# Kernel tuning notes

Hardware: AMD Instinct MI355X
Metric: run time of the kernel (lower is better)

Reference implementation:

```python
import jax, jax.numpy as jnp
import numpy as np

D = 1024        # input_dim == hidden_dim (residual add requires equality)
NUM_CLASSES = 2
EPS = 1e-5      # torch LayerNorm default


def _layer_norm(x, gamma, beta):
    mu = jnp.mean(x, axis=-1, keepdims=True)
    var = jnp.var(x, axis=-1, keepdims=True)
    return (x - mu) * jax.lax.rsqrt(var + EPS) * gamma + beta


def setup_inputs() -> dict:
    key = jax.random.key(0)
    ks = jax.random.split(key, 16)
    B, S = 8, 2048
    s = 1.0 / np.sqrt(D)
    inp = {
        "x": jax.random.normal(ks[0], (B, S, D), dtype=jnp.float32),
        "Wq": jax.random.normal(ks[1], (D, D), dtype=jnp.float32) * s,
        "bq": jnp.zeros((D,), jnp.float32),
        "Wk": jax.random.normal(ks[2], (D, D), dtype=jnp.float32) * s,
        "bk": jnp.zeros((D,), jnp.float32),
        "Wv": jax.random.normal(ks[3], (D, D), dtype=jnp.float32) * s,
        "bv": jnp.zeros((D,), jnp.float32),
        "Wd": jax.random.normal(ks[4], (D, D), dtype=jnp.float32) * s,
        "bd": jnp.zeros((D,), jnp.float32),
        "g1": jnp.ones((D,), jnp.float32),
        "b1": jnp.zeros((D,), jnp.float32),
        "g2": jnp.ones((D,), jnp.float32),
        "b2": jnp.zeros((D,), jnp.float32),
        "Wc": jax.random.normal(ks[5], (D, NUM_CLASSES), dtype=jnp.float32) * s,
        "bc": jnp.zeros((NUM_CLASSES,), jnp.float32),
    }
    return inp


def reference(x, Wq, bq, Wk, bk, Wv, bv, Wd, bd, g1, b1, g2, b2, Wc, bc):
    # Q/K/V projections
    q = x @ Wq + bq                                   # [B,S,D]
    k = x @ Wk + bk
    v = x @ Wv + bv
    # scores scaled by sqrt(input_dim) (as in the original code)
    scores = jnp.einsum('bsd,btd->bst', q, k) / np.sqrt(D).astype(np.float32)
    attn = jax.nn.softmax(scores, axis=-1)            # [B,S,S]
    weighted = jnp.einsum('bst,btd->bsd', attn, v)    # [B,S,D]
    weighted = _layer_norm(weighted + x, g1, b1)
    h = jax.nn.relu(weighted @ Wd + bd)
    h = _layer_norm(h + weighted, g2, b2)
    # dropout is identity in eval mode
    logits = h[:, 0, :] @ Wc + bc                     # [B,num_classes]
    return logits
```

## Files before the change

### kernel.cpp

```cpp
#include <hip/hip_runtime.h>
#include <math.h>

#define B 8
#define S 2048
#define D 1024

__device__ __forceinline__ float waveReduceSum(float v) {
#pragma unroll
    for (int k = 32; k >= 1; k >>= 1) v += __shfl_xor(v, k, 64);
    return v;
}
__device__ __forceinline__ float waveReduceMax(float v) {
#pragma unroll
    for (int k = 32; k >= 1; k >>= 1) v = fmaxf(v, __shfl_xor(v, k, 64));
    return v;
}
__device__ float blockReduceSum(float v) {
    __shared__ float sm[4];
    int lane = threadIdx.x & 63, wid = threadIdx.x >> 6;
    v = waveReduceSum(v);
    __syncthreads();
    if (lane == 0) sm[wid] = v;
    __syncthreads();
    return sm[0] + sm[1] + sm[2] + sm[3];
}

__global__ void __launch_bounds__(256) k1_q0(const float* __restrict__ x,
                                             const float* __restrict__ Wq,
                                             const float* __restrict__ bq,
                                             float* __restrict__ q0,
                                             float* __restrict__ zero_region) {
    const int tid = threadIdx.x;
    zero_region[blockIdx.x * 256 + tid] = 0.f;

    const int dp0 = blockIdx.x * 16;
    const int dpl = tid & 15, kg = tid >> 4;
    __shared__ float xs[8][1024];
    for (int j = tid; j < 2048; j += 256) {
        int b = j >> 8, off = j & 255;
        ((float4*)xs[b])[off] = ((const float4*)(x + (size_t)b * S * D))[off];
    }
    __syncthreads();
    float acc[8] = {0.f, 0.f, 0.f, 0.f, 0.f, 0.f, 0.f, 0.f};
    const int k0 = kg * 64;
    for (int i = 0; i < 64; ++i) {
        int k = k0 + i;
        float wv = Wq[(size_t)k * D + dp0 + dpl];
#pragma unroll
        for (int b = 0; b < 8; ++b) acc[b] += xs[b][k] * wv;
    }
    __shared__ float red[16 * 16 * 9];
#pragma unroll
    for (int b = 0; b < 8; ++b) red[(kg * 16 + dpl) * 9 + b] = acc[b];
    __syncthreads();
    if (tid < 128) {
        int dpl2 = tid >> 3, b = tid & 7;
        float s = 0.f;
#pragma unroll
        for (int g = 0; g < 16; ++g) s += red[(g * 16 + dpl2) * 9 + b];
        q0[b * D + dp0 + dpl2] = s + bq[dp0 + dpl2];
    }
}

__global__ void __launch_bounds__(256) k2_u(const float* __restrict__ Wk,
                                            const float* __restrict__ q0,
                                            float* __restrict__ u) {
    int wid = (blockIdx.x * 256 + threadIdx.x) >> 6;
    int lane = threadIdx.x & 63;
    const float4* Wk4 = (const float4*)(Wk + (size_t)wid * D);
    const float4* q04 = (const float4*)q0;
    float acc[8] = {0.f, 0.f, 0.f, 0.f, 0.f, 0.f, 0.f, 0.f};
#pragma unroll
    for (int i = 0; i < 4; ++i) {
        float4 wv = Wk4[lane + 64 * i];
#pragma unroll
        for (int b = 0; b < 8; ++b) {
            float4 qv = q04[b * 256 + lane + 64 * i];
            acc[b] += wv.x * qv.x + wv.y * qv.y + wv.z * qv.z + wv.w * qv.w;
        }
    }
#pragma unroll
    for (int b = 0; b < 8; ++b) {
        float v = waveReduceSum(acc[b]);
        if (lane == 0) u[b * D + wid] = v;
    }
}

__global__ void __launch_bounds__(256) k3_attn(const float* __restrict__ x,
                                               const float* __restrict__ u,
                                               float* __restrict__ pml,
                                               float* __restrict__ pw) {
    const int b = blockIdx.y;
    const int t0 = blockIdx.x * 16;
    const int tid = threadIdx.x;
    const int wave = tid >> 6, lane = tid & 63;
    const float4* xb4 = (const float4*)(x + (size_t)b * S * D);
    float4 xr[16];
#pragma unroll
    for (int t = 0; t < 16; ++t) xr[t] = xb4[(size_t)(t0 + t) * 256 + tid];
    float4 uv = ((const float4*)(u + b * D))[tid];
    __shared__ float part[16][256];
#pragma unroll
    for (int t = 0; t < 16; ++t)
        part[t][tid] = xr[t].x * uv.x + xr[t].y * uv.y + xr[t].z * uv.z + xr[t].w * uv.w;
    __syncthreads();
    __shared__ float s_sc[16];
#pragma unroll
    for (int r = 0; r < 4; ++r) {
        int t = wave * 4 + r;
        float v = part[t][lane] + part[t][lane + 64] + part[t][lane + 128] + part[t][lane + 192];
        v = waveReduceSum(v);
        if (lane == 0) s_sc[t] = v * 0.03125f;
    }
    __syncthreads();
    float m = -INFINITY;
#pragma unroll
    for (int t = 0; t < 16; ++t) m = fmaxf(m, s_sc[t]);
    float p[16], l = 0.f;
#pragma unroll
    for (int t = 0; t < 16; ++t) {
        p[t] = __expf(s_sc[t] - m);
        l += p[t];
    }
    float4 wl = {0.f, 0.f, 0.f, 0.f};
#pragma unroll
    for (int t = 0; t < 16; ++t) {
        wl.x += p[t] * xr[t].x;
        wl.y += p[t] * xr[t].y;
        wl.z += p[t] * xr[t].z;
        wl.w += p[t] * xr[t].w;
    }
    const int pidx = b * 128 + blockIdx.x;
    ((float4*)(pw + (size_t)pidx * 1024))[tid] = wl;
    if (tid == 0) {
        pml[pidx * 2 + 0] = m;
        pml[pidx * 2 + 1] = l;
    }
}

__global__ void __launch_bounds__(256) k4_comb_wv(const float* __restrict__ pml,
                                                  const float* __restrict__ pw,
                                                  const float* __restrict__ Wv,
                                                  float* __restrict__ wacc) {
    const int tid = threadIdx.x;
    const int bid = blockIdx.x;
    const int d0 = (bid >> 2) * 32;
    const int dp = (bid & 3) * 256 + tid;
    const int wave = tid >> 6, lane = tid & 63;
    __shared__ float pm[8][128], pl[8][128], sc[8][128];
    __shared__ float sM[8], sL[8];
    __shared__ float vs[8][32];
    for (int j = tid; j < 1024; j += 256) {
        int b = j >> 7, blk = j & 127;
        pm[b][blk] = pml[(b * 128 + blk) * 2 + 0];
        pl[b][blk] = pml[(b * 128 + blk) * 2 + 1];
    }
    __syncthreads();
#pragma unroll
    for (int h = 0; h < 2; ++h) {
        int b = wave + h * 4;
        float mv = fmaxf(pm[b][lane], pm[b][lane + 64]);
        float M = waveReduceMax(mv);
        float lp = __expf(pm[b][lane] - M) * pl[b][lane] +
                   __expf(pm[b][lane + 64] - M) * pl[b][lane + 64];
        float L = waveReduceSum(lp);
        if (lane == 0) {
            sM[b] = M;
            sL[b] = L;
        }
    }
    __syncthreads();
    for (int j = tid; j < 1024; j += 256) {
        int b = j >> 7, blk = j & 127;
        sc[b][blk] = __expf(pm[b][blk] - sM[b]);
    }
    __syncthreads();
    {
        int b = tid >> 5, dd = tid & 31, d = d0 + dd;
        float acc = 0.f;
#pragma unroll 4
        for (int blk = 0; blk < 128; ++blk)
            acc += sc[b][blk] * pw[(size_t)(b * 128 + blk) * 1024 + d];
        vs[b][dd] = acc / sL[b];
    }
    __syncthreads();
    float acc[8] = {0.f, 0.f, 0.f, 0.f, 0.f, 0.f, 0.f, 0.f};
#pragma unroll 4
    for (int dd = 0; dd < 32; ++dd) {
        float wv = Wv[(size_t)(d0 + dd) * D + dp];
#pragma unroll
        for (int b = 0; b < 8; ++b) acc[b] += vs[b][dd] * wv;
    }
#pragma unroll
    for (int b = 0; b < 8; ++b) atomicAdd(&wacc[b * D + dp], acc[b]);
}

__global__ void __launch_bounds__(256) k5_ln1_wd(const float* __restrict__ wacc,
                                                 const float* __restrict__ bv,
                                                 const float* __restrict__ x,
                                                 const float* __restrict__ g1,
                                                 const float* __restrict__ b1,
                                                 const float* __restrict__ Wd,
                                                 float* __restrict__ hacc) {
    const int tid = threadIdx.x;
    const int bid = blockIdx.x;
    const int d0 = (bid >> 2) * 32;
    const int dp = (bid & 3) * 256 + tid;
    const int wave = tid >> 6, lane = tid & 63;
    __shared__ float sMu[8], sInv[8], vs[8][32];
    {
        const float4* wacc4 = (const float4*)wacc;
        const float4* bv4 = (const float4*)bv;
#pragma unroll
        for (int h = 0; h < 2; ++h) {
            int b = wave + h * 4;
            const float4* xb4r = (const float4*)(x + (size_t)b * S * D);
            float s = 0.f, ss = 0.f;
#pragma unroll
            for (int i = 0; i < 4; ++i) {
                int idx = lane + 64 * i;
                float4 wv = wacc4[b * 256 + idx];
                float4 bb = bv4[idx];
                float4 xv = xb4r[idx];
                float v0 = wv.x + bb.x + xv.x;
                float v1 = wv.y + bb.y + xv.y;
                float v2 = wv.z + bb.z + xv.z;
                float v3 = wv.w + bb.w + xv.w;
                s += v0 + v1 + v2 + v3;
                ss += v0 * v0 + v1 * v1 + v2 * v2 + v3 * v3;
            }
            s = waveReduceSum(s);
            ss = waveReduceSum(ss);
            if (lane == 0) {
                float mu = s * (1.0f / D);
                sMu[b] = mu;
                sInv[b] = rsqrtf(ss * (1.0f / D) - mu * mu + 1e-5f);
            }
        }
    }
    __syncthreads();
    {
        int b = tid >> 5, dd = tid & 31, d = d0 + dd;
        float v = wacc[b * D + d] + bv[d] + x[(size_t)b * S * D + d];
        vs[b][dd] = (v - sMu[b]) * sInv[b] * g1[d] + b1[d];
    }
    __syncthreads();
    float acc[8] = {0.f, 0.f, 0.f, 0.f, 0.f, 0.f, 0.f, 0.f};
#pragma unroll 4
    for (int dd = 0; dd < 32; ++dd) {
        float wv = Wd[(size_t)(d0 + dd) * D + dp];
#pragma unroll
        for (int b = 0; b < 8; ++b) acc[b] += vs[b][dd] * wv;
    }
#pragma unroll
    for (int b = 0; b < 8; ++b) atomicAdd(&hacc[b * D + dp], acc[b]);
}

__global__ void __launch_bounds__(256) k6_final(const float* __restrict__ wacc,
                                                const float* __restrict__ bv,
                                                const float* __restrict__ x,
                                                const float* __restrict__ g1,
                                                const float* __restrict__ b1,
                                                const float* __restrict__ hacc,
                                                const float* __restrict__ bd,
                                                const float* __restrict__ g2,
                                                const float* __restrict__ b2,
                                                const float* __restrict__ Wc,
                                                const float* __restrict__ bc,
                                                float* __restrict__ out) {
    const int b = blockIdx.x;
    const int tid = threadIdx.x;
    float r[4];
    float s = 0.f, ss = 0.f;
#pragma unroll
    for (int i = 0; i < 4; ++i) {
        int e = tid * 4 + i;
        float v = wacc[b * D + e] + bv[e] + x[(size_t)b * S * D + e];
        r[i] = v;
        s += v;
        ss += v * v;
    }
    s = blockReduceSum(s);
    ss = blockReduceSum(ss);
    float mu1 = s * (1.0f / D);
    float inv1 = rsqrtf(ss * (1.0f / D) - mu1 * mu1 + 1e-5f);
    float t[4];
    float s2 = 0.f, ss2 = 0.f;
#pragma unroll
    for (int i = 0; i < 4; ++i) {
        int e = tid * 4 + i;
        float ln1v = (r[i] - mu1) * inv1 * g1[e] + b1[e];
        float h = fmaxf(hacc[b * D + e] + bd[e], 0.f) + ln1v;
        t[i] = h;
        s2 += h;
        ss2 += h * h;
    }
    s2 = blockReduceSum(s2);
    ss2 = blockReduceSum(ss2);
    float mu2 = s2 * (1.0f / D);
    float inv2 = rsqrtf(ss2 * (1.0f / D) - mu2 * mu2 + 1e-5f);
    float p0 = 0.f, p1 = 0.f;
#pragma unroll
    for (int i = 0; i < 4; ++i) {
        int e = tid * 4 + i;
        float l2 = (t[i] - mu2) * inv2 * g2[e] + b2[e];
        p0 += l2 * Wc[e * 2 + 0];
        p1 += l2 * Wc[e * 2 + 1];
    }
    p0 = blockReduceSum(p0);
    p1 = blockReduceSum(p1);
    if (tid == 0) {
        out[b * 2 + 0] = p0 + bc[0];
        out[b * 2 + 1] = p1 + bc[1];
    }
}

extern "C" void kernel_launch(void* const* d_in, const int* in_sizes, int n_in,
                              void* d_out, int out_size, void* d_ws, size_t ws_size,
                              hipStream_t stream) {
    const float* x  = (const float*)d_in[0];
    const float* Wq = (const float*)d_in[1];
    const float* bq = (const float*)d_in[2];
    const float* Wk = (const float*)d_in[3];
    const float* Wv = (const float*)d_in[5];
    const float* bv = (const float*)d_in[6];
    const float* Wd = (const float*)d_in[7];
    const float* bd = (const float*)d_in[8];
    const float* g1 = (const float*)d_in[9];
    const float* b1 = (const float*)d_in[10];
    const float* g2 = (const float*)d_in[11];
    const float* b2 = (const float*)d_in[12];
    const float* Wc = (const float*)d_in[13];
    const float* bc = (const float*)d_in[14];
    float* out = (float*)d_out;

    float* ws   = (float*)d_ws;
    float* q0   = ws;
    float* u    = ws + 8192;
    float* wacc = ws + 16384;
    float* hacc = ws + 24576;
    float* pml  = ws + 32768;
    float* pw   = ws + 34816;

    k1_q0<<<64, 256, 0, stream>>>(x, Wq, bq, q0, wacc);
    k2_u<<<256, 256, 0, stream>>>(Wk, q0, u);
    k3_attn<<<dim3(128, 8), 256, 0, stream>>>(x, u, pml, pw);
    k4_comb_wv<<<128, 256, 0, stream>>>(pml, pw, Wv, wacc);
    k5_ln1_wd<<<128, 256, 0, stream>>>(wacc, bv, x, g1, b1, Wd, hacc);
    k6_final<<<8, 256, 0, stream>>>(wacc, bv, x, g1, b1, hacc, bd, g2, b2, Wc, bc, out);
}
```

Before: 167.1 us.

## Fuse all six stage kernels into one persistent kernel with grid barriers

Replaces the six sequential kernel launches with a single persistent kernel of 256 blocks that loops over virtual block indices for each stage. Stages are separated by software grid barriers built from atomic counters and flags, and all per-stage shared memory is packed into one union. The aim is to remove launch overhead and the inter-kernel gaps. In exchange the attention stage, previously 1024 blocks, now runs as several passes per block, and correctness depends on all 256 blocks being co-resident. The barrier spin has a timeout break that could silently desynchronize stages.

New measurement: 485.5 us. 2.9x slower.

```diff
diff --git a/kernel.cpp b/kernel.cpp
--- a/kernel.cpp
+++ b/kernel.cpp
@@ -4,6 +4,7 @@
 #define B 8
 #define S 2048
 #define D 1024
+#define NB 256
 
 __device__ __forceinline__ float waveReduceSum(float v) {
 #pragma unroll
@@ -25,17 +26,42 @@
     return sm[0] + sm[1] + sm[2] + sm[3];
 }
 
-__global__ void __launch_bounds__(256) k1_q0(const float* __restrict__ x,
-                                             const float* __restrict__ Wq,
-                                             const float* __restrict__ bq,
-                                             float* __restrict__ q0,
-                                             float* __restrict__ zero_region) {
-    const int tid = threadIdx.x;
-    zero_region[blockIdx.x * 256 + tid] = 0.f;
-
-    const int dp0 = blockIdx.x * 16;
+__device__ __forceinline__ void gbar(unsigned* cnt, unsigned* flag) {
+    __threadfence();
+    __syncthreads();
+    if (threadIdx.x == 0) {
+        unsigned a = atomicAdd(cnt, 1u);
+        if (a == NB - 1u) {
+            __threadfence();
+            __hip_atomic_store(flag, 1u, __ATOMIC_RELEASE,
+                               __HIP_MEMORY_SCOPE_AGENT);
+        } else {
+            long spins = 0;
+            while (__hip_atomic_load(flag, __ATOMIC_ACQUIRE,
+                                     __HIP_MEMORY_SCOPE_AGENT) == 0u) {
+                __builtin_amdgcn_s_sleep(1);
+                if (++spins > (1L << 24)) break;
+            }
+        }
+    }
+    __syncthreads();
+    __threadfence();
+}
+
+struct P3S { float part[16][256]; float s_sc[16]; };
+struct P4S { float pm[8][128]; float pl[8][128]; float sc[8][128];
+             float sM[8]; float sL[8]; float vs[8][32]; };
+struct P5S { float sMu[8]; float sInv[8]; float vs[8][32]; };
+union ShU { float xs[8192]; P3S p3; P4S p4; P5S p5; };
+
+
+__device__ __forceinline__ void body_q0(int vb, int tid,
+        const float* __restrict__ x, const float* __restrict__ Wq,
+        const float* __restrict__ bq, float* __restrict__ q0,
+        float* shbuf) {
+    const int dp0 = vb * 16;
     const int dpl = tid & 15, kg = tid >> 4;
-    __shared__ float xs[8][1024];
+    float (*xs)[1024] = (float(*)[1024])shbuf;
     for (int j = tid; j < 2048; j += 256) {
         int b = j >> 8, off = j & 255;
         ((float4*)xs[b])[off] = ((const float4*)(x + (size_t)b * S * D))[off];
@@ -49,7 +75,8 @@
 #pragma unroll
         for (int b = 0; b < 8; ++b) acc[b] += xs[b][k] * wv;
     }
-    __shared__ float red[16 * 16 * 9];
+    __syncthreads();
+    float* red = shbuf;
 #pragma unroll
     for (int b = 0; b < 8; ++b) red[(kg * 16 + dpl) * 9 + b] = acc[b];
     __syncthreads();
@@ -60,13 +87,14 @@
         for (int g = 0; g < 16; ++g) s += red[(g * 16 + dpl2) * 9 + b];
         q0[b * D + dp0 + dpl2] = s + bq[dp0 + dpl2];
     }
-}
-
-__global__ void __launch_bounds__(256) k2_u(const float* __restrict__ Wk,
-                                            const float* __restrict__ q0,
-                                            float* __restrict__ u) {
-    int wid = (blockIdx.x * 256 + threadIdx.x) >> 6;
-    int lane = threadIdx.x & 63;
+    __syncthreads();
+}
+
+__device__ __forceinline__ void body_u(int vb, int tid,
+        const float* __restrict__ Wk, const float* __restrict__ q0,
+        float* __restrict__ u) {
+    int wid = (vb * 256 + tid) >> 6;
+    int lane = tid & 63;
     const float4* Wk4 = (const float4*)(Wk + (size_t)wid * D);
     const float4* q04 = (const float4*)q0;
     float acc[8] = {0.f, 0.f, 0.f, 0.f, 0.f, 0.f, 0.f, 0.f};
@@ -86,93 +114,83 @@
     }
 }
 
-__global__ void __launch_bounds__(256) k3_attn(const float* __restrict__ x,
-                                               const float* __restrict__ u,
-                                               float* __restrict__ pml,
-                                               float* __restrict__ pw) {
-    const int b = blockIdx.y;
-    const int t0 = blockIdx.x * 16;
-    const int tid = threadIdx.x;
+__device__ __forceinline__ void body_attn(int vb, int tid,
+        const float* __restrict__ x, const float* __restrict__ u,
+        float* __restrict__ pml, float* __restrict__ pw, P3S* p3) {
+    const int b = vb >> 7;
+    const int bx = vb & 127;
+    const int t0 = bx * 16;
     const int wave = tid >> 6, lane = tid & 63;
     const float4* xb4 = (const float4*)(x + (size_t)b * S * D);
     float4 xr[16];
 #pragma unroll
     for (int t = 0; t < 16; ++t) xr[t] = xb4[(size_t)(t0 + t) * 256 + tid];
     float4 uv = ((const float4*)(u + b * D))[tid];
-    __shared__ float part[16][256];
 #pragma unroll
     for (int t = 0; t < 16; ++t)
-        part[t][tid] = xr[t].x * uv.x + xr[t].y * uv.y + xr[t].z * uv.z + xr[t].w * uv.w;
-    __syncthreads();
-    __shared__ float s_sc[16];
+        p3->part[t][tid] = xr[t].x * uv.x + xr[t].y * uv.y + xr[t].z * uv.z + xr[t].w * uv.w;
+    __syncthreads();
 #pragma unroll
     for (int r = 0; r < 4; ++r) {
         int t = wave * 4 + r;
-        float v = part[t][lane] + part[t][lane + 64] + part[t][lane + 128] + part[t][lane + 192];
+        float v = p3->part[t][lane] + p3->part[t][lane + 64] +
+                  p3->part[t][lane + 128] + p3->part[t][lane + 192];
         v = waveReduceSum(v);
-        if (lane == 0) s_sc[t] = v * 0.03125f;
+        if (lane == 0) p3->s_sc[t] = v * 0.03125f;
     }
     __syncthreads();
     float m = -INFINITY;
 #pragma unroll
-    for (int t = 0; t < 16; ++t) m = fmaxf(m, s_sc[t]);
-    float p[16], l = 0.f;
+    for (int t = 0; t < 16; ++t) m = fmaxf(m, p3->s_sc[t]);
+    float l = 0.f;
+    float4 wl = {0.f, 0.f, 0.f, 0.f};
 #pragma unroll
     for (int t = 0; t < 16; ++t) {
-        p[t] = __expf(s_sc[t] - m);
-        l += p[t];
-    }
-    float4 wl = {0.f, 0.f, 0.f, 0.f};
-#pragma unroll
-    for (int t = 0; t < 16; ++t) {
-        wl.x += p[t] * xr[t].x;
-        wl.y += p[t] * xr[t].y;
-        wl.z += p[t] * xr[t].z;
-        wl.w += p[t] * xr[t].w;
-    }
-    const int pidx = b * 128 + blockIdx.x;
+        float p = __expf(p3->s_sc[t] - m);
+        l += p;
+        wl.x += p * xr[t].x;
+        wl.y += p * xr[t].y;
+        wl.z += p * xr[t].z;
+        wl.w += p * xr[t].w;
+    }
+    const int pidx = b * 128 + bx;
     ((float4*)(pw + (size_t)pidx * 1024))[tid] = wl;
     if (tid == 0) {
         pml[pidx * 2 + 0] = m;
         pml[pidx * 2 + 1] = l;
     }
-}
-
-__global__ void __launch_bounds__(256) k4_comb_wv(const float* __restrict__ pml,
-                                                  const float* __restrict__ pw,
-                                                  const float* __restrict__ Wv,
-                                                  float* __restrict__ wacc) {
-    const int tid = threadIdx.x;
-    const int bid = blockIdx.x;
-    const int d0 = (bid >> 2) * 32;
-    const int dp = (bid & 3) * 256 + tid;
+    __syncthreads();
+}
+
+__device__ __forceinline__ void body_comb_wv(int vb, int tid,
+        const float* __restrict__ pml, const float* __restrict__ pw,
+        const float* __restrict__ Wv, float* __restrict__ wacc, P4S* p4) {
+    const int d0 = (vb >> 2) * 32;
+    const int dp = (vb & 3) * 256 + tid;
     const int wave = tid >> 6, lane = tid & 63;
-    __shared__ float pm[8][128], pl[8][128], sc[8][128];
-    __shared__ float sM[8], sL[8];
-    __shared__ float vs[8][32];
     for (int j = tid; j < 1024; j += 256) {
         int b = j >> 7, blk = j & 127;
-        pm[b][blk] = pml[(b * 128 + blk) * 2 + 0];
-        pl[b][blk] = pml[(b * 128 + blk) * 2 + 1];
+        p4->pm[b][blk] = pml[(b * 128 + blk) * 2 + 0];
+        p4->pl[b][blk] = pml[(b * 128 + blk) * 2 + 1];
     }
     __syncthreads();
 #pragma unroll
     for (int h = 0; h < 2; ++h) {
         int b = wave + h * 4;
-        float mv = fmaxf(pm[b][lane], pm[b][lane + 64]);
+        float mv = fmaxf(p4->pm[b][lane], p4->pm[b][lane + 64]);
         float M = waveReduceMax(mv);
-        float lp = __expf(pm[b][lane] - M) * pl[b][lane] +
-                   __expf(pm[b][lane + 64] - M) * pl[b][lane + 64];
+        float lp = __expf(p4->pm[b][lane] - M) * p4->pl[b][lane] +
+                   __expf(p4->pm[b][lane + 64] - M) * p4->pl[b][lane + 64];
         float L = waveReduceSum(lp);
         if (lane == 0) {
-            sM[b] = M;
-            sL[b] = L;
+            p4->sM[b] = M;
+            p4->sL[b] = L;
         }
     }
     __syncthreads();
     for (int j = tid; j < 1024; j += 256) {
         int b = j >> 7, blk = j & 127;
-        sc[b][blk] = __expf(pm[b][blk] - sM[b]);
+        p4->sc[b][blk] = __expf(p4->pm[b][blk] - p4->sM[b]);
     }
     __syncthreads();
     {
@@ -180,8 +198,8 @@
         float acc = 0.f;
 #pragma unroll 4
         for (int blk = 0; blk < 128; ++blk)
-            acc += sc[b][blk] * pw[(size_t)(b * 128 + blk) * 1024 + d];
-        vs[b][dd] = acc / sL[b];
+            acc += p4->sc[b][blk] * pw[(size_t)(b * 128 + blk) * 1024 + d];
+        p4->vs[b][dd] = acc / p4->sL[b];
     }
     __syncthreads();
     float acc[8] = {0.f, 0.f, 0.f, 0.f, 0.f, 0.f, 0.f, 0.f};
@@ -189,25 +207,21 @@
     for (int dd = 0; dd < 32; ++dd) {
         float wv = Wv[(size_t)(d0 + dd) * D + dp];
 #pragma unroll
-        for (int b = 0; b < 8; ++b) acc[b] += vs[b][dd] * wv;
+        for (int b = 0; b < 8; ++b) acc[b] += p4->vs[b][dd] * wv;
     }
 #pragma unroll
     for (int b = 0; b < 8; ++b) atomicAdd(&wacc[b * D + dp], acc[b]);
-}
-
-__global__ void __launch_bounds__(256) k5_ln1_wd(const float* __restrict__ wacc,
-                                                 const float* __restrict__ bv,
-                                                 const float* __restrict__ x,
-                                                 const float* __restrict__ g1,
-                                                 const float* __restrict__ b1,
-                                                 const float* __restrict__ Wd,
-                                                 float* __restrict__ hacc) {
-    const int tid = threadIdx.x;
-    const int bid = blockIdx.x;
-    const int d0 = (bid >> 2) * 32;
-    const int dp = (bid & 3) * 256 + tid;
+    __syncthreads();
+}
+
+__device__ __forceinline__ void body_ln1_wd(int vb, int tid,
+        const float* __restrict__ wacc, const float* __restrict__ bv,
+        const float* __restrict__ x, const float* __restrict__ g1,
+        const float* __restrict__ b1, const float* __restrict__ Wd,
+        float* __restrict__ hacc, P5S* p5) {
+    const int d0 = (vb >> 2) * 32;
+    const int dp = (vb & 3) * 256 + tid;
     const int wave = tid >> 6, lane = tid & 63;
-    __shared__ float sMu[8], sInv[8], vs[8][32];
     {
         const float4* wacc4 = (const float4*)wacc;
         const float4* bv4 = (const float4*)bv;
@@ -233,8 +247,8 @@
             ss = waveReduceSum(ss);
             if (lane == 0) {
                 float mu = s * (1.0f / D);
-                sMu[b] = mu;
-                sInv[b] = rsqrtf(ss * (1.0f / D) - mu * mu + 1e-5f);
+                p5->sMu[b] = mu;
+                p5->sInv[b] = rsqrtf(ss * (1.0f / D) - mu * mu + 1e-5f);
             }
         }
     }
@@ -242,7 +256,7 @@
     {
         int b = tid >> 5, dd = tid & 31, d = d0 + dd;
         float v = wacc[b * D + d] + bv[d] + x[(size_t)b * S * D + d];
-        vs[b][dd] = (v - sMu[b]) * sInv[b] * g1[d] + b1[d];
+        p5->vs[b][dd] = (v - p5->sMu[b]) * p5->sInv[b] * g1[d] + b1[d];
     }
     __syncthreads();
     float acc[8] = {0.f, 0.f, 0.f, 0.f, 0.f, 0.f, 0.f, 0.f};
@@ -250,26 +264,20 @@
     for (int dd = 0; dd < 32; ++dd) {
         float wv = Wd[(size_t)(d0 + dd) * D + dp];
 #pragma unroll
-        for (int b = 0; b < 8; ++b) acc[b] += vs[b][dd] * wv;
+        for (int b = 0; b < 8; ++b) acc[b] += p5->vs[b][dd] * wv;
     }
 #pragma unroll
     for (int b = 0; b < 8; ++b) atomicAdd(&hacc[b * D + dp], acc[b]);
-}
-
-__global__ void __launch_bounds__(256) k6_final(const float* __restrict__ wacc,
-                                                const float* __restrict__ bv,
-                                                const float* __restrict__ x,
-                                                const float* __restrict__ g1,
-                                                const float* __restrict__ b1,
-                                                const float* __restrict__ hacc,
-                                                const float* __restrict__ bd,
-                                                const float* __restrict__ g2,
-                                                const float* __restrict__ b2,
-                                                const float* __restrict__ Wc,
-                                                const float* __restrict__ bc,
-                                                float* __restrict__ out) {
-    const int b = blockIdx.x;
-    const int tid = threadIdx.x;
+    __syncthreads();
+}
+
+__device__ __forceinline__ void body_final(int b, int tid,
+        const float* __restrict__ wacc, const float* __restrict__ bv,
+        const float* __restrict__ x, const float* __restrict__ g1,
+        const float* __restrict__ b1, const float* __restrict__ hacc,
+        const float* __restrict__ bd, const float* __restrict__ g2,
+        const float* __restrict__ b2, const float* __restrict__ Wc,
+        const float* __restrict__ bc, float* __restrict__ out) {
     float r[4];
     float s = 0.f, ss = 0.f;
 #pragma unroll
@@ -313,6 +321,55 @@
         out[b * 2 + 0] = p0 + bc[0];
         out[b * 2 + 1] = p1 + bc[1];
     }
+    __syncthreads();
+}
+
+#define BAR_OFF 1083392
+
+__global__ void k_init(unsigned* bars) {
+    if (threadIdx.x < 16) bars[threadIdx.x] = 0u;
+}
+
+__global__ void __launch_bounds__(256) fused_all(
+        const float* __restrict__ x,
+        const float* __restrict__ Wq, const float* __restrict__ bq,
+        const float* __restrict__ Wk,
+        const float* __restrict__ Wv, const float* __restrict__ bv,
+        const float* __restrict__ Wd, const float* __restrict__ bd,
+        const float* __restrict__ g1, const float* __restrict__ b1,
+        const float* __restrict__ g2, const float* __restrict__ b2,
+        const float* __restrict__ Wc, const float* __restrict__ bc,
+        float* __restrict__ out, float* __restrict__ ws) {
+    float* q0   = ws;
+    float* u    = ws + 8192;
+    float* wacc = ws + 16384;
+    float* hacc = ws + 24576;
+    float* pml  = ws + 32768;
+    float* pw   = ws + 34816;
+    unsigned* bars = (unsigned*)(ws + BAR_OFF);
+
+    const int tid = threadIdx.x;
+    __shared__ ShU sh;
+
+    for (int i = blockIdx.x * 256 + tid; i < 16384; i += NB * 256) wacc[i] = 0.f;
+
+    for (int vb = blockIdx.x; vb < 64; vb += NB)
+        body_q0(vb, tid, x, Wq, bq, q0, sh.xs);
+    gbar(&bars[0], &bars[1]);
+    for (int vb = blockIdx.x; vb < 256; vb += NB)
+        body_u(vb, tid, Wk, q0, u);
+    gbar(&bars[2], &bars[3]);
+    for (int vb = blockIdx.x; vb < 1024; vb += NB)
+        body_attn(vb, tid, x, u, pml, pw, &sh.p3);
+    gbar(&bars[4], &bars[5]);
+    for (int vb = blockIdx.x; vb < 128; vb += NB)
+        body_comb_wv(vb, tid, pml, pw, Wv, wacc, &sh.p4);
+    gbar(&bars[6], &bars[7]);
+    for (int vb = blockIdx.x; vb < 128; vb += NB)
+        body_ln1_wd(vb, tid, wacc, bv, x, g1, b1, Wd, hacc, &sh.p5);
+    gbar(&bars[8], &bars[9]);
+    for (int vb = blockIdx.x; vb < 8; vb += NB)
+        body_final(vb, tid, wacc, bv, x, g1, b1, hacc, bd, g2, b2, Wc, bc, out);
 }
 
 extern "C" void kernel_launch(void* const* d_in, const int* in_sizes, int n_in,
@@ -333,19 +390,9 @@
     const float* Wc = (const float*)d_in[13];
     const float* bc = (const float*)d_in[14];
     float* out = (float*)d_out;
-
-    float* ws   = (float*)d_ws;
-    float* q0   = ws;
-    float* u    = ws + 8192;
-    float* wacc = ws + 16384;
-    float* hacc = ws + 24576;
-    float* pml  = ws + 32768;
-    float* pw   = ws + 34816;
-
-    k1_q0<<<64, 256, 0, stream>>>(x, Wq, bq, q0, wacc);
-    k2_u<<<256, 256, 0, stream>>>(Wk, q0, u);
-    k3_attn<<<dim3(128, 8), 256, 0, stream>>>(x, u, pml, pw);
-    k4_comb_wv<<<128, 256, 0, stream>>>(pml, pw, Wv, wacc);
-    k5_ln1_wd<<<128, 256, 0, stream>>>(wacc, bv, x, g1, b1, Wd, hacc);
-    k6_final<<<8, 256, 0, stream>>>(wacc, bv, x, g1, b1, hacc, bd, g2, b2, Wc, bc, out);
-}
+    float* ws = (float*)d_ws;
+
+    k_init<<<1, 64, 0, stream>>>((unsigned*)(ws + BAR_OFF));
+    fused_all<<<NB, 256, 0, stream>>>(x, Wq, bq, Wk, Wv, bv, Wd, bd,
+                                      g1, b1, g2, b2, Wc, bc, out, ws);
+}
```
